# Performance work log

Hardware: AMD Instinct MI355X
Metric: run time of the kernel (lower is better)

The kernel has to match this reference:

```python
import jax, jax.numpy as jnp
import numpy as np

N = 100000   # nodes
E = 1600000  # edges (avg degree 16)
Q = 64       # mesoscale velocity bins
H = 64       # collision MLP hidden dim
DT = 0.1
REG = 1e-6


def setup_inputs() -> dict:
    key = jax.random.key(0)
    ks = jax.random.split(key, 10)
    return {
        "f": jax.random.uniform(ks[0], (N, Q), jnp.float32),
        "macro_u": jax.random.normal(ks[1], (N, 1), jnp.float32),
        "source": 0.01 * jax.random.normal(ks[2], (N, Q), jnp.float32),
        "edge_src": jax.random.randint(ks[3], (E,), 0, N, jnp.int32),
        "edge_dst": jax.random.randint(ks[4], (E,), 0, N, jnp.int32),
        "edge_w": jax.random.uniform(ks[5], (E,), jnp.float32),
        "xi": jnp.linspace(-1.0, 1.0, Q).astype(jnp.float32),
        "w_in": jax.random.normal(ks[6], (Q, H), jnp.float32) / np.float32(np.sqrt(Q)),
        "b_in": jnp.zeros((H,), jnp.float32),
        "w_hid": jax.random.normal(ks[7], (3, H, H), jnp.float32) / np.float32(np.sqrt(H)),
        "b_hid": jnp.zeros((3, H), jnp.float32),
        "w_out": jax.random.normal(ks[8], (H, Q), jnp.float32) / np.float32(np.sqrt(H)),
        "b_out": jnp.zeros((Q,), jnp.float32),
    }


def _collision(f, macro_u, xi, w_in, b_in, w_hid, b_hid, w_out, b_out):
    # 5-layer MLP: relu hidden, tanh output (CollisionOperator.forward)
    x = jax.nn.relu(f @ w_in + b_in)
    for i in range(3):  # fixed small layer count, not a data-dim loop
        x = jax.nn.relu(x @ w_hid[i] + b_hid[i])
    omega = jnp.tanh(x @ w_out + b_out)                     # [N, Q]
    # Hard collision-invariance constraint: Omega* = (I - C^T (C C^T)^-1 C) Omega
    q = f.shape[1]
    w = jnp.full((q,), 1.0 / q, f.dtype)                    # quadrature weights
    xi_shifted = xi[None, :] + macro_u                      # [N, Q]
    C = jnp.stack([jnp.broadcast_to(w, xi_shifted.shape), w * xi_shifted], axis=1)  # [N,2,Q]
    CCT = jnp.einsum('naq,nbq->nab', C, C) + REG * jnp.eye(2, dtype=f.dtype)        # [N,2,2]
    v = jnp.einsum('naq,nq->na', C, omega)                  # [N,2]
    s = jnp.linalg.solve(CCT, v[..., None])[..., 0]         # [N,2]  (== CCT^-1 v)
    return omega - jnp.einsum('naq,na->nq', C, s)           # avoid dense [N,Q,Q] projection


def _transport(f, xi, edge_src, edge_dst, edge_w, n):
    # BoltzmannUpdater.compute_transport_term: both inflow (on graph) and
    # outflow (on reverse graph) reduce to the same per-edge message
    #   m_e = (w_e / out_deg[src_e]) * xi * (f[dst_e] - f[src_e])
    # aggregated at dst (inflow) and at src (outflow); transport = outflow - inflow.
    out_deg = jax.ops.segment_sum(jnp.ones_like(edge_w), edge_src, num_segments=n)
    q_e = edge_w / out_deg[edge_src]                         # [E]
    msg = q_e[:, None] * xi[None, :] * (f[edge_dst] - f[edge_src])  # [E, Q]
    inflow = jax.ops.segment_sum(msg, edge_dst, num_segments=n)
    outflow = jax.ops.segment_sum(msg, edge_src, num_segments=n)
    return outflow - inflow


def reference(f, macro_u, source, edge_src, edge_dst, edge_w, xi,
              w_in, b_in, w_hid, b_hid, w_out, b_out):
    f = jnp.maximum(f, 0.0)  # clamp(min=0)
    omega = _collision(f, macro_u, xi, w_in, b_in, w_hid, b_hid, w_out, b_out)
    trans = _transport(f, xi, edge_src, edge_dst, edge_w, f.shape[0])
    f_new = f - DT * (trans - omega - source)
    return jnp.maximum(f_new, 0.0)
```

## Files before the change

kernel.cpp:

```cpp
#include <hip/hip_runtime.h>

#define NN 100000
#define EE 1600000
#define DTc 0.1f
#define REGc 1e-6f
#define WQc (1.0f / 64.0f)

#define NB 782
#define CHUNK 2048
#define NCH 782
#define SC_NB 598
#define MPAD (SC_NB * 1024)
#define TENT (2 * EE)
#define ACT_S 72
#define PRE_NB 6250
#define WP_NB 80
#define SIDE_BIT (1u << 24)

typedef unsigned long long u64;
typedef __attribute__((ext_vector_type(8))) short short8;
typedef __attribute__((ext_vector_type(4))) float f32x4;

__device__ __forceinline__ unsigned short f2bf(float x) {
    unsigned u = __float_as_uint(x);
    unsigned r = (u + 0x7fffu + ((u >> 16) & 1u)) >> 16;
    return (unsigned short)r;
}
__device__ __forceinline__ float bf2f(unsigned short s) {
    return __uint_as_float(((unsigned)s) << 16);
}

__global__ __launch_bounds__(256) void prep_kernel(
    const float* __restrict__ f, unsigned int* __restrict__ fb16u,
    const float* __restrict__ w_in, const float* __restrict__ w_hid,
    const float* __restrict__ w_out, unsigned short* __restrict__ wp,
    const int* __restrict__ esrc, const int* __restrict__ edst,
    int* __restrict__ bc) {
    int b = blockIdx.x;
    if (b < NCH) {
        __shared__ int cnt[NB];
        int t = threadIdx.x;
        for (int j = t; j < NB; j += 256) cnt[j] = 0;
        __syncthreads();
        int base = b * CHUNK;
        int nE = min(CHUNK, EE - base);
        int i = t * 8;
        if (i < nE) {
            int4 sa = *(const int4*)&esrc[base + i];
            int4 sb = *(const int4*)&esrc[base + i + 4];
            int4 da = *(const int4*)&edst[base + i];
            int4 db = *(const int4*)&edst[base + i + 4];
            atomicAdd(&cnt[sa.x >> 7], 1); atomicAdd(&cnt[da.x >> 7], 1);
            atomicAdd(&cnt[sa.y >> 7], 1); atomicAdd(&cnt[da.y >> 7], 1);
            atomicAdd(&cnt[sa.z >> 7], 1); atomicAdd(&cnt[da.z >> 7], 1);
            atomicAdd(&cnt[sa.w >> 7], 1); atomicAdd(&cnt[da.w >> 7], 1);
            atomicAdd(&cnt[sb.x >> 7], 1); atomicAdd(&cnt[db.x >> 7], 1);
            atomicAdd(&cnt[sb.y >> 7], 1); atomicAdd(&cnt[db.y >> 7], 1);
            atomicAdd(&cnt[sb.z >> 7], 1); atomicAdd(&cnt[db.z >> 7], 1);
            atomicAdd(&cnt[sb.w >> 7], 1); atomicAdd(&cnt[db.w >> 7], 1);
        }
        __syncthreads();
        for (int j = t; j < NB; j += 256) bc[j * NCH + b] = cnt[j];
    } else if (b < NCH + PRE_NB) {
        int i = (b - NCH) * 256 + threadIdx.x;
        float4 v = *(const float4*)&f[i * 4];
        unsigned lo = (unsigned)f2bf(fmaxf(v.x, 0.f)) | ((unsigned)f2bf(fmaxf(v.y, 0.f)) << 16);
        unsigned hi = (unsigned)f2bf(fmaxf(v.z, 0.f)) | ((unsigned)f2bf(fmaxf(v.w, 0.f)) << 16);
        fb16u[i * 2] = lo;
        fb16u[i * 2 + 1] = hi;
    } else {
        int i = (b - NCH - PRE_NB) * 256 + threadIdx.x;
        int l = i >> 12, idx = i & 4095;
        int n = idx >> 6, k = idx & 63;
        const float* W = (l == 0) ? w_in : (l < 4 ? w_hid + (l - 1) * 4096 : w_out);
        wp[i] = f2bf(W[k * 64 + n]);
    }
}

__global__ __launch_bounds__(1024) void scan_blocks(int* __restrict__ data,
                                                    int* __restrict__ bsums) {
    __shared__ int s[1024];
    int t = threadIdx.x;
    int i = blockIdx.x * 1024 + t;
    int v = data[i];
    s[t] = v;
    __syncthreads();
    for (int o = 1; o < 1024; o <<= 1) {
        int x = (t >= o) ? s[t - o] : 0;
        __syncthreads();
        s[t] += x;
        __syncthreads();
    }
    data[i] = s[t] - v;
    if (t == 0) bsums[blockIdx.x] = s[1023];
}

__global__ __launch_bounds__(1024) void scan_sums(int* __restrict__ bsums) {
    __shared__ int s[1024];
    int t = threadIdx.x;
    int v = (t < SC_NB) ? bsums[t] : 0;
    s[t] = v;
    __syncthreads();
    for (int o = 1; o < 1024; o <<= 1) {
        int x = (t >= o) ? s[t - o] : 0;
        __syncthreads();
        s[t] += x;
        __syncthreads();
    }
    if (t < SC_NB) bsums[t] = s[t] - v;
}

__global__ __launch_bounds__(256) void bin_scatter(
    const int* __restrict__ esrc, const int* __restrict__ edst,
    const float* __restrict__ ew,
    const int* __restrict__ offs, const int* __restrict__ bsums,
    u64* __restrict__ adj64) {
    __shared__ int cur[NB];
    int t = threadIdx.x, blk = blockIdx.x;
    for (int j = t; j < NB; j += 256) {
        int idx = j * NCH + blk;
        cur[j] = offs[idx] + bsums[idx >> 10];
    }
    __syncthreads();
    int base = blk * CHUNK;
    int nE = min(CHUNK, EE - base);
    int i = t * 8;
    if (i < nE) {
        int4 sa = *(const int4*)&esrc[base + i];
        int4 sb = *(const int4*)&esrc[base + i + 4];
        int4 da = *(const int4*)&edst[base + i];
        int4 db = *(const int4*)&edst[base + i + 4];
        float4 wa = *(const float4*)&ew[base + i];
        float4 wb = *(const float4*)&ew[base + i + 4];
#define EMIT(s, d, w)                                                         \
        {                                                                     \
            u64 wb64 = ((u64)__float_as_uint(w)) << 32;                       \
            int p1 = atomicAdd(&cur[(s) >> 7], 1);                            \
            adj64[p1] = wb64 | SIDE_BIT | (unsigned)((d) | (((s) & 127) << 17)); \
            int p2 = atomicAdd(&cur[(d) >> 7], 1);                            \
            adj64[p2] = wb64 | (unsigned)((s) | (((d) & 127) << 17));         \
        }
        EMIT(sa.x, da.x, wa.x) EMIT(sa.y, da.y, wa.y)
        EMIT(sa.z, da.z, wa.z) EMIT(sa.w, da.w, wa.w)
        EMIT(sb.x, db.x, wb.x) EMIT(sb.y, db.y, wb.y)
        EMIT(sb.z, db.z, wb.z) EMIT(sb.w, db.w, wb.w)
#undef EMIT
    }
}

__global__ __launch_bounds__(256) void bucket_histo(
    const int* __restrict__ offs, const int* __restrict__ bsums,
    const u64* __restrict__ adj64,
    int* __restrict__ node_offs, int* __restrict__ deg) {
    __shared__ int cnt_tot[128], cnt_src[128], sc[128];
    int t = threadIdx.x, b = blockIdx.x;
    if (t < 128) { cnt_tot[t] = 0; cnt_src[t] = 0; }
    __syncthreads();
    int i0 = b * NCH;
    int i1 = (b + 1) * NCH;
    int start = offs[i0] + bsums[i0 >> 10];
    int end = offs[i1] + bsums[i1 >> 10];
    for (int i = start + t; i < end; i += 256) {
        unsigned lo = (unsigned)adj64[i];
        int local = (lo >> 17) & 127;
        atomicAdd(&cnt_tot[local], 1);
        if (lo & SIDE_BIT) atomicAdd(&cnt_src[local], 1);
    }
    __syncthreads();
    if (t < 128) sc[t] = cnt_tot[t];
    __syncthreads();
    for (int o = 1; o < 128; o <<= 1) {
        int x = 0;
        if (t < 128 && t >= o) x = sc[t - o];
        __syncthreads();
        if (t < 128) sc[t] += x;
        __syncthreads();
    }
    if (t < 128) {
        int n = b * 128 + t;
        if (n < NN) {
            node_offs[n] = start + sc[t] - cnt_tot[t];
            deg[n] = cnt_src[t];
        }
    }
    if (b == 0 && t == 0) node_offs[NN] = TENT;
}

__global__ __launch_bounds__(256) void bucket_scatter(
    const int* __restrict__ offs, const int* __restrict__ bsums,
    const u64* __restrict__ adj64, const int* __restrict__ node_offs,
    const int* __restrict__ deg, unsigned int* __restrict__ adj4) {
    __shared__ int cur[128];
    __shared__ float ldeg[128];
    int t = threadIdx.x, b = blockIdx.x;
    if (t < 128) {
        int n = b * 128 + t;
        cur[t] = (n < NN) ? node_offs[n] : 0;
        ldeg[t] = (n < NN) ? (float)deg[n] : 1.f;
    }
    __syncthreads();
    int i0 = b * NCH;
    int i1 = (b + 1) * NCH;
    int start = offs[i0] + bsums[i0 >> 10];
    int end = offs[i1] + bsums[i1 >> 10];
    for (int i = start + t; i < end; i += 256) {
        u64 e = adj64[i];
        unsigned lo = (unsigned)e;
        int local = (lo >> 17) & 127;
        unsigned other = lo & 0x1FFFFu;
        float w = __uint_as_float((unsigned)(e >> 32));
        float dv = (lo & SIDE_BIT) ? ldeg[local] : (float)deg[other];
        float q = w / dv;
        unsigned q15 = (unsigned)(q * 32768.f + 0.5f);
        if (q15 > 32767u) q15 = 32767u;
        int p = atomicAdd(&cur[local], 1);
        adj4[p] = (q15 << 17) | other;
    }
}

#define ACC8(q, r)                                          \
    a0 = fmaf(q, __uint_as_float(r.x << 16), a0);           \
    a1 = fmaf(q, __uint_as_float(r.x & 0xFFFF0000u), a1);   \
    a2 = fmaf(q, __uint_as_float(r.y << 16), a2);           \
    a3 = fmaf(q, __uint_as_float(r.y & 0xFFFF0000u), a3);   \
    a4 = fmaf(q, __uint_as_float(r.z << 16), a4);           \
    a5 = fmaf(q, __uint_as_float(r.z & 0xFFFF0000u), a5);   \
    a6 = fmaf(q, __uint_as_float(r.w << 16), a6);           \
    a7 = fmaf(q, __uint_as_float(r.w & 0xFFFF0000u), a7);   \
    qs += q;

__global__ __launch_bounds__(256) void gather_kernel(
    const unsigned int* __restrict__ fb16u, const int* __restrict__ node_offs,
    const unsigned int* __restrict__ adj, const float* __restrict__ xi,
    float* __restrict__ trans) {
    const float QS = 1.f / 32768.f;
    int lane = threadIdx.x & 63;
    int n = blockIdx.x * 4 + (threadIdx.x >> 6);
    if (n >= NN) return;
    int c = lane & 7;
    int qt = lane >> 3;
    int j = node_offs[n];
    int end = node_offs[n + 1];
    float a0 = 0.f, a1 = 0.f, a2 = 0.f, a3 = 0.f;
    float a4 = 0.f, a5 = 0.f, a6 = 0.f, a7 = 0.f, qs = 0.f;
    for (; j + 32 <= end; j += 32) {
        unsigned e0 = __builtin_nontemporal_load(&adj[j + qt]);
        unsigned e1 = __builtin_nontemporal_load(&adj[j + 8 + qt]);
        unsigned e2 = __builtin_nontemporal_load(&adj[j + 16 + qt]);
        unsigned e3 = __builtin_nontemporal_load(&adj[j + 24 + qt]);
        uint4 r0 = *(const uint4*)&fb16u[(e0 & 0x1FFFFu) * 32 + c * 4];
        uint4 r1 = *(const uint4*)&fb16u[(e1 & 0x1FFFFu) * 32 + c * 4];
        uint4 r2 = *(const uint4*)&fb16u[(e2 & 0x1FFFFu) * 32 + c * 4];
        uint4 r3 = *(const uint4*)&fb16u[(e3 & 0x1FFFFu) * 32 + c * 4];
        float q0 = (float)(e0 >> 17) * QS;
        float q1 = (float)(e1 >> 17) * QS;
        float q2 = (float)(e2 >> 17) * QS;
        float q3 = (float)(e3 >> 17) * QS;
        ACC8(q0, r0)
        ACC8(q1, r1)
        ACC8(q2, r2)
        ACC8(q3, r3)
    }
    for (; j + 8 <= end; j += 8) {
        unsigned e = __builtin_nontemporal_load(&adj[j + qt]);
        uint4 r = *(const uint4*)&fb16u[(e & 0x1FFFFu) * 32 + c * 4];
        float q = (float)(e >> 17) * QS;
        ACC8(q, r)
    }
    if (j < end) {
        int idx = j + qt;
        bool ok = idx < end;
        unsigned e = ok ? adj[idx] : 0u;
        uint4 r = *(const uint4*)&fb16u[(e & 0x1FFFFu) * 32 + c * 4];
        float q = ok ? (float)(e >> 17) * QS : 0.f;
        ACC8(q, r)
    }
#define RED3(x) x += __shfl_xor(x, 8); x += __shfl_xor(x, 16); x += __shfl_xor(x, 32)
    RED3(a0); RED3(a1); RED3(a2); RED3(a3);
    RED3(a4); RED3(a5); RED3(a6); RED3(a7); RED3(qs);
    if (qt == 0) {
        uint4 rn = *(const uint4*)&fb16u[n * 32 + c * 4];
        float4 x0 = *(const float4*)&xi[c * 8];
        float4 x1 = *(const float4*)&xi[c * 8 + 4];
        f32x4 o0, o1;
        o0.x = x0.x * (a0 - qs * __uint_as_float(rn.x << 16));
        o0.y = x0.y * (a1 - qs * __uint_as_float(rn.x & 0xFFFF0000u));
        o0.z = x0.z * (a2 - qs * __uint_as_float(rn.y << 16));
        o0.w = x0.w * (a3 - qs * __uint_as_float(rn.y & 0xFFFF0000u));
        o1.x = x1.x * (a4 - qs * __uint_as_float(rn.z << 16));
        o1.y = x1.y * (a5 - qs * __uint_as_float(rn.z & 0xFFFF0000u));
        o1.z = x1.z * (a6 - qs * __uint_as_float(rn.w << 16));
        o1.w = x1.w * (a7 - qs * __uint_as_float(rn.w & 0xFFFF0000u));
        __builtin_nontemporal_store(o0, (f32x4*)&trans[n * 64 + c * 8]);
        __builtin_nontemporal_store(o1, (f32x4*)&trans[n * 64 + c * 8 + 4]);
    }
}

__global__ __launch_bounds__(256) void node_kernel(
    const unsigned short* __restrict__ fb16, const float* __restrict__ f,
    const float* __restrict__ macro_u, const float* __restrict__ source,
    const float* __restrict__ xi, const unsigned short* __restrict__ wp,
    const float* __restrict__ b_in, const float* __restrict__ b_hid,
    const float* __restrict__ b_out,
    const float* __restrict__ trans, float* __restrict__ out) {
    __shared__ __attribute__((aligned(16))) unsigned short act[128 * ACT_S];
    __shared__ float s0s[128], s1s[128], us[128], xif[64];

    const int t = threadIdx.x;
    const int wid = t >> 6;
    const int lane = t & 63;
    const int m = lane & 15;
    const int quad = lane >> 4;
    const int nodeBase = blockIdx.x * 128;
    const int gbase = nodeBase * 64;

    if (t < 128) {
        int n = nodeBase + t;
        us[t] = (n < NN) ? macro_u[n] : 0.f;
    }
    if (t < 64) xif[t] = xi[t];

#pragma unroll
    for (int i = 0; i < 8; i++) {
        int r = wid * 32 + i * 4 + (lane >> 4);
        int c = (lane & 15) * 4;
        uint2 v = {0u, 0u};
        if (nodeBase + r < NN) v = *(const uint2*)&fb16[gbase + r * 64 + c];
        *(uint2*)&act[r * ACT_S + c] = v;
    }

    const int rowbase = wid * 32;

    for (int l = 0; l < 5; l++) {
        const unsigned short* W = wp + l * 4096;
        const float* B = (l == 0) ? b_in : (l < 4 ? b_hid + (l - 1) * 64 : b_out);

        short8 Af[2][2], Bf[4][2];
#pragma unroll
        for (int rt = 0; rt < 2; rt++)
#pragma unroll
            for (int kk = 0; kk < 2; kk++)
                Af[rt][kk] = *(const short8*)&act[(rowbase + rt * 16 + m) * ACT_S + kk * 32 + quad * 8];
#pragma unroll
        for (int ct = 0; ct < 4; ct++)
#pragma unroll
            for (int kk = 0; kk < 2; kk++)
                Bf[ct][kk] = *(const short8*)&W[(ct * 16 + m) * 64 + kk * 32 + quad * 8];

        f32x4 acc[2][4];
#pragma unroll
        for (int rt = 0; rt < 2; rt++)
#pragma unroll
            for (int ct = 0; ct < 4; ct++) {
                acc[rt][ct] = (f32x4){0.f, 0.f, 0.f, 0.f};
                acc[rt][ct] = __builtin_amdgcn_mfma_f32_16x16x32_bf16(Af[rt][0], Bf[ct][0], acc[rt][ct], 0, 0, 0);
                acc[rt][ct] = __builtin_amdgcn_mfma_f32_16x16x32_bf16(Af[rt][1], Bf[ct][1], acc[rt][ct], 0, 0, 0);
            }

#pragma unroll
        for (int rt = 0; rt < 2; rt++)
#pragma unroll
            for (int ct = 0; ct < 4; ct++) {
                float bv = B[ct * 16 + m];
#pragma unroll
                for (int r = 0; r < 4; r++) {
                    int row = rowbase + rt * 16 + quad * 4 + r;
                    float val = acc[rt][ct][r] + bv;
                    val = (l < 4) ? fmaxf(val, 0.f) : tanhf(val);
                    act[row * ACT_S + ct * 16 + m] = f2bf(val);
                }
            }
    }
    __syncthreads();

    if (t < 128) {
        float u = us[t];
        float v0 = 0.f, v1 = 0.f, sxs2 = 0.f, sxi = 0.f;
        const short8* rp = (const short8*)&act[t * ACT_S];
#pragma unroll
        for (int c = 0; c < 8; c++) {
            short8 v = rp[c];
#pragma unroll
            for (int jj = 0; jj < 8; jj++) {
                float om = bf2f((unsigned short)v[jj]);
                float xv = xif[c * 8 + jj];
                float xs = xv + u;
                v0 += om;
                v1 += xs * om;
                sxs2 += xs * xs;
                sxi += xv;
            }
        }
        v0 *= WQc;
        v1 *= WQc;
        float c00 = WQc + REGc;
        float c01 = WQc * WQc * (sxi + 64.f * u);
        float c11 = WQc * WQc * sxs2 + REGc;
        float det = c00 * c11 - c01 * c01;
        float inv = 1.0f / det;
        s0s[t] = (c11 * v0 - c01 * v1) * inv;
        s1s[t] = (c00 * v1 - c01 * v0) * inv;
    }
    __syncthreads();

#pragma unroll
    for (int i = 0; i < 8; i++) {
        int e = (i * 256 + t) * 4;
        int nl = e >> 6;
        if (nodeBase + nl < NN) {
            int g = gbase + e;
            int c0 = e & 63;
            float4 fv = *(const float4*)&f[g];
            float4 sv = *(const float4*)&source[g];
            float4 tv = *(const float4*)&trans[g];
            float uu = us[nl];
            float sv0 = s0s[nl], sv1 = s1s[nl];
            float4 ov;
            float* ovp = (float*)&ov;
            const float* fp = (const float*)&fv;
            const float* sp = (const float*)&sv;
            const float* tp = (const float*)&tv;
#pragma unroll
            for (int jj = 0; jj < 4; jj++) {
                float om = bf2f(act[nl * ACT_S + c0 + jj]);
                float xs = xif[c0 + jj] + uu;
                float omst = om - WQc * (sv0 + xs * sv1);
                float val = fmaxf(fp[jj], 0.f) + DTc * (sp[jj] + omst - tp[jj]);
                ovp[jj] = fmaxf(val, 0.f);
            }
            *(float4*)&out[g] = ov;
        }
    }
}

extern "C" void kernel_launch(void* const* d_in, const int* in_sizes, int n_in,
                              void* d_out, int out_size, void* d_ws, size_t ws_size,
                              hipStream_t stream) {
    const float* f       = (const float*)d_in[0];
    const float* macro_u = (const float*)d_in[1];
    const float* source  = (const float*)d_in[2];
    const int*   esrc    = (const int*)d_in[3];
    const int*   edst    = (const int*)d_in[4];
    const float* ew      = (const float*)d_in[5];
    const float* xi      = (const float*)d_in[6];
    const float* w_in    = (const float*)d_in[7];
    const float* b_in    = (const float*)d_in[8];
    const float* w_hid   = (const float*)d_in[9];
    const float* b_hid   = (const float*)d_in[10];
    const float* w_out   = (const float*)d_in[11];
    const float* b_out   = (const float*)d_in[12];
    float* out = (float*)d_out;

    u64* adj64 = (u64*)d_ws;
    unsigned int* adj4 = (unsigned int*)(adj64 + TENT);
    int* deg   = (int*)(adj4 + TENT);
    int* bc    = deg + NN;
    int* bsums = bc + MPAD;
    int* node_offs = bsums + 1024;
    float* trans = (float*)(node_offs + NN + 8);
    unsigned short* fb16 = (unsigned short*)(trans + (size_t)NN * 64);
    unsigned short* wp = fb16 + (size_t)NN * 64;

    hipMemsetAsync(bc, 0, (size_t)MPAD * sizeof(int), stream);

    prep_kernel<<<NCH + PRE_NB + WP_NB, 256, 0, stream>>>(
        f, (unsigned int*)fb16, w_in, w_hid, w_out, wp, esrc, edst, bc);
    scan_blocks<<<SC_NB, 1024, 0, stream>>>(bc, bsums);
    scan_sums<<<1, 1024, 0, stream>>>(bsums);
    bin_scatter<<<NCH, 256, 0, stream>>>(esrc, edst, ew, bc, bsums, adj64);
    bucket_histo<<<NB, 256, 0, stream>>>(bc, bsums, adj64, node_offs, deg);
    bucket_scatter<<<NB, 256, 0, stream>>>(bc, bsums, adj64, node_offs, deg, adj4);
    gather_kernel<<<(NN + 3) / 4, 256, 0, stream>>>((const unsigned int*)fb16,
                                                    node_offs, adj4, xi, trans);
    node_kernel<<<(NN + 127) / 128, 256, 0, stream>>>(
        fb16, f, macro_u, source, xi, wp, b_in, b_hid, b_out, trans, out);
}
```

Before: 336.4 us.

## Replace global bin-count scan with fixed-capacity buckets and atomic bucket cursors

Removes the separate per-chunk histogram pass, the 600K-entry memset and the two-level scan. bin_scatter now counts locally, reserves space in each 128-node bucket via one global atomic per bucket, and writes into fixed-capacity (CAP) slots; a single small scan over 782 bucket totals yields compact offsets for node_offs. The bf16 prep also writes 16-byte vectors. Risk: a bucket exceeding CAP entries would overflow, and edge order within buckets becomes nondeterministic.

New measurement: 336.8 us. No clear change (+0.1%).

```diff
diff --git a/kernel.cpp b/kernel.cpp
--- a/kernel.cpp
+++ b/kernel.cpp
@@ -7,13 +7,11 @@
 #define WQc (1.0f / 64.0f)
 
 #define NB 782
-#define CHUNK 2048
-#define NCH 782
-#define SC_NB 598
-#define MPAD (SC_NB * 1024)
+#define CAP 4736
+#define BS_NB 782
 #define TENT (2 * EE)
 #define ACT_S 72
-#define PRE_NB 6250
+#define PRE_NB 3125
 #define WP_NB 80
 #define SIDE_BIT (1u << 24)
 
@@ -29,47 +27,27 @@
 __device__ __forceinline__ float bf2f(unsigned short s) {
     return __uint_as_float(((unsigned)s) << 16);
 }
+__device__ __forceinline__ unsigned pack2(float a, float b) {
+    return (unsigned)f2bf(fmaxf(a, 0.f)) | ((unsigned)f2bf(fmaxf(b, 0.f)) << 16);
+}
 
 __global__ __launch_bounds__(256) void prep_kernel(
     const float* __restrict__ f, unsigned int* __restrict__ fb16u,
     const float* __restrict__ w_in, const float* __restrict__ w_hid,
-    const float* __restrict__ w_out, unsigned short* __restrict__ wp,
-    const int* __restrict__ esrc, const int* __restrict__ edst,
-    int* __restrict__ bc) {
+    const float* __restrict__ w_out, unsigned short* __restrict__ wp) {
     int b = blockIdx.x;
-    if (b < NCH) {
-        __shared__ int cnt[NB];
-        int t = threadIdx.x;
-        for (int j = t; j < NB; j += 256) cnt[j] = 0;
-        __syncthreads();
-        int base = b * CHUNK;
-        int nE = min(CHUNK, EE - base);
-        int i = t * 8;
-        if (i < nE) {
-            int4 sa = *(const int4*)&esrc[base + i];
-            int4 sb = *(const int4*)&esrc[base + i + 4];
-            int4 da = *(const int4*)&edst[base + i];
-            int4 db = *(const int4*)&edst[base + i + 4];
-            atomicAdd(&cnt[sa.x >> 7], 1); atomicAdd(&cnt[da.x >> 7], 1);
-            atomicAdd(&cnt[sa.y >> 7], 1); atomicAdd(&cnt[da.y >> 7], 1);
-            atomicAdd(&cnt[sa.z >> 7], 1); atomicAdd(&cnt[da.z >> 7], 1);
-            atomicAdd(&cnt[sa.w >> 7], 1); atomicAdd(&cnt[da.w >> 7], 1);
-            atomicAdd(&cnt[sb.x >> 7], 1); atomicAdd(&cnt[db.x >> 7], 1);
-            atomicAdd(&cnt[sb.y >> 7], 1); atomicAdd(&cnt[db.y >> 7], 1);
-            atomicAdd(&cnt[sb.z >> 7], 1); atomicAdd(&cnt[db.z >> 7], 1);
-            atomicAdd(&cnt[sb.w >> 7], 1); atomicAdd(&cnt[db.w >> 7], 1);
-        }
-        __syncthreads();
-        for (int j = t; j < NB; j += 256) bc[j * NCH + b] = cnt[j];
-    } else if (b < NCH + PRE_NB) {
-        int i = (b - NCH) * 256 + threadIdx.x;
-        float4 v = *(const float4*)&f[i * 4];
-        unsigned lo = (unsigned)f2bf(fmaxf(v.x, 0.f)) | ((unsigned)f2bf(fmaxf(v.y, 0.f)) << 16);
-        unsigned hi = (unsigned)f2bf(fmaxf(v.z, 0.f)) | ((unsigned)f2bf(fmaxf(v.w, 0.f)) << 16);
-        fb16u[i * 2] = lo;
-        fb16u[i * 2 + 1] = hi;
+    if (b < PRE_NB) {
+        int i = b * 256 + threadIdx.x;
+        float4 v0 = *(const float4*)&f[i * 8];
+        float4 v1 = *(const float4*)&f[i * 8 + 4];
+        uint4 w;
+        w.x = pack2(v0.x, v0.y);
+        w.y = pack2(v0.z, v0.w);
+        w.z = pack2(v1.x, v1.y);
+        w.w = pack2(v1.z, v1.w);
+        *(uint4*)&fb16u[i * 4] = w;
     } else {
-        int i = (b - NCH - PRE_NB) * 256 + threadIdx.x;
+        int i = (b - PRE_NB) * 256 + threadIdx.x;
         int l = i >> 12, idx = i & 4095;
         int n = idx >> 6, k = idx & 63;
         const float* W = (l == 0) ? w_in : (l < 4 ? w_hid + (l - 1) * 4096 : w_out);
@@ -77,67 +55,51 @@
     }
 }
 
-__global__ __launch_bounds__(1024) void scan_blocks(int* __restrict__ data,
-                                                    int* __restrict__ bsums) {
-    __shared__ int s[1024];
-    int t = threadIdx.x;
-    int i = blockIdx.x * 1024 + t;
-    int v = data[i];
-    s[t] = v;
-    __syncthreads();
-    for (int o = 1; o < 1024; o <<= 1) {
-        int x = (t >= o) ? s[t - o] : 0;
-        __syncthreads();
-        s[t] += x;
-        __syncthreads();
-    }
-    data[i] = s[t] - v;
-    if (t == 0) bsums[blockIdx.x] = s[1023];
-}
-
-__global__ __launch_bounds__(1024) void scan_sums(int* __restrict__ bsums) {
-    __shared__ int s[1024];
-    int t = threadIdx.x;
-    int v = (t < SC_NB) ? bsums[t] : 0;
-    s[t] = v;
-    __syncthreads();
-    for (int o = 1; o < 1024; o <<= 1) {
-        int x = (t >= o) ? s[t - o] : 0;
-        __syncthreads();
-        s[t] += x;
-        __syncthreads();
-    }
-    if (t < SC_NB) bsums[t] = s[t] - v;
-}
-
 __global__ __launch_bounds__(256) void bin_scatter(
     const int* __restrict__ esrc, const int* __restrict__ edst,
-    const float* __restrict__ ew,
-    const int* __restrict__ offs, const int* __restrict__ bsums,
+    const float* __restrict__ ew, int* __restrict__ bcur,
     u64* __restrict__ adj64) {
-    __shared__ int cur[NB];
+    __shared__ int cnt[NB];
+    __shared__ int bas[NB];
     int t = threadIdx.x, blk = blockIdx.x;
+    for (int j = t; j < NB; j += 256) cnt[j] = 0;
+    __syncthreads();
+    int base = blk * 2048;
+    int nE = min(2048, EE - base);
+    int i = t * 8;
+    bool act = (i < nE);
+    int4 sa, sb, da, db;
+    float4 wa, wb;
+    if (act) {
+        sa = *(const int4*)&esrc[base + i];
+        sb = *(const int4*)&esrc[base + i + 4];
+        da = *(const int4*)&edst[base + i];
+        db = *(const int4*)&edst[base + i + 4];
+        wa = *(const float4*)&ew[base + i];
+        wb = *(const float4*)&ew[base + i + 4];
+        atomicAdd(&cnt[sa.x >> 7], 1); atomicAdd(&cnt[da.x >> 7], 1);
+        atomicAdd(&cnt[sa.y >> 7], 1); atomicAdd(&cnt[da.y >> 7], 1);
+        atomicAdd(&cnt[sa.z >> 7], 1); atomicAdd(&cnt[da.z >> 7], 1);
+        atomicAdd(&cnt[sa.w >> 7], 1); atomicAdd(&cnt[da.w >> 7], 1);
+        atomicAdd(&cnt[sb.x >> 7], 1); atomicAdd(&cnt[db.x >> 7], 1);
+        atomicAdd(&cnt[sb.y >> 7], 1); atomicAdd(&cnt[db.y >> 7], 1);
+        atomicAdd(&cnt[sb.z >> 7], 1); atomicAdd(&cnt[db.z >> 7], 1);
+        atomicAdd(&cnt[sb.w >> 7], 1); atomicAdd(&cnt[db.w >> 7], 1);
+    }
+    __syncthreads();
     for (int j = t; j < NB; j += 256) {
-        int idx = j * NCH + blk;
-        cur[j] = offs[idx] + bsums[idx >> 10];
-    }
-    __syncthreads();
-    int base = blk * CHUNK;
-    int nE = min(CHUNK, EE - base);
-    int i = t * 8;
-    if (i < nE) {
-        int4 sa = *(const int4*)&esrc[base + i];
-        int4 sb = *(const int4*)&esrc[base + i + 4];
-        int4 da = *(const int4*)&edst[base + i];
-        int4 db = *(const int4*)&edst[base + i + 4];
-        float4 wa = *(const float4*)&ew[base + i];
-        float4 wb = *(const float4*)&ew[base + i + 4];
+        int c = cnt[j];
+        bas[j] = (c ? atomicAdd(&bcur[j], c) : 0) + j * CAP;
+        cnt[j] = 0;
+    }
+    __syncthreads();
+    if (act) {
 #define EMIT(s, d, w)                                                         \
         {                                                                     \
             u64 wb64 = ((u64)__float_as_uint(w)) << 32;                       \
-            int p1 = atomicAdd(&cur[(s) >> 7], 1);                            \
+            int p1 = bas[(s) >> 7] + atomicAdd(&cnt[(s) >> 7], 1);            \
             adj64[p1] = wb64 | SIDE_BIT | (unsigned)((d) | (((s) & 127) << 17)); \
-            int p2 = atomicAdd(&cur[(d) >> 7], 1);                            \
+            int p2 = bas[(d) >> 7] + atomicAdd(&cnt[(d) >> 7], 1);            \
             adj64[p2] = wb64 | (unsigned)((s) | (((d) & 127) << 17));         \
         }
         EMIT(sa.x, da.x, wa.x) EMIT(sa.y, da.y, wa.y)
@@ -148,20 +110,34 @@
     }
 }
 
+__global__ __launch_bounds__(1024) void scan_nb(const int* __restrict__ bcur,
+                                                int* __restrict__ cbase) {
+    __shared__ int s[1024];
+    int t = threadIdx.x;
+    int v = (t < NB) ? bcur[t] : 0;
+    s[t] = v;
+    __syncthreads();
+    for (int o = 1; o < 1024; o <<= 1) {
+        int x = (t >= o) ? s[t - o] : 0;
+        __syncthreads();
+        s[t] += x;
+        __syncthreads();
+    }
+    if (t < NB) cbase[t] = s[t] - v;
+}
+
 __global__ __launch_bounds__(256) void bucket_histo(
-    const int* __restrict__ offs, const int* __restrict__ bsums,
+    const int* __restrict__ bcur, const int* __restrict__ cbase,
     const u64* __restrict__ adj64,
     int* __restrict__ node_offs, int* __restrict__ deg) {
     __shared__ int cnt_tot[128], cnt_src[128], sc[128];
     int t = threadIdx.x, b = blockIdx.x;
     if (t < 128) { cnt_tot[t] = 0; cnt_src[t] = 0; }
     __syncthreads();
-    int i0 = b * NCH;
-    int i1 = (b + 1) * NCH;
-    int start = offs[i0] + bsums[i0 >> 10];
-    int end = offs[i1] + bsums[i1 >> 10];
-    for (int i = start + t; i < end; i += 256) {
-        unsigned lo = (unsigned)adj64[i];
+    int used = bcur[b];
+    int gstart = b * CAP;
+    for (int i = t; i < used; i += 256) {
+        unsigned lo = (unsigned)adj64[gstart + i];
         int local = (lo >> 17) & 127;
         atomicAdd(&cnt_tot[local], 1);
         if (lo & SIDE_BIT) atomicAdd(&cnt_src[local], 1);
@@ -179,7 +155,7 @@
     if (t < 128) {
         int n = b * 128 + t;
         if (n < NN) {
-            node_offs[n] = start + sc[t] - cnt_tot[t];
+            node_offs[n] = cbase[b] + sc[t] - cnt_tot[t];
             deg[n] = cnt_src[t];
         }
     }
@@ -187,9 +163,9 @@
 }
 
 __global__ __launch_bounds__(256) void bucket_scatter(
-    const int* __restrict__ offs, const int* __restrict__ bsums,
-    const u64* __restrict__ adj64, const int* __restrict__ node_offs,
-    const int* __restrict__ deg, unsigned int* __restrict__ adj4) {
+    const int* __restrict__ bcur, const u64* __restrict__ adj64,
+    const int* __restrict__ node_offs, const int* __restrict__ deg,
+    unsigned int* __restrict__ adj4) {
     __shared__ int cur[128];
     __shared__ float ldeg[128];
     int t = threadIdx.x, b = blockIdx.x;
@@ -199,12 +175,10 @@
         ldeg[t] = (n < NN) ? (float)deg[n] : 1.f;
     }
     __syncthreads();
-    int i0 = b * NCH;
-    int i1 = (b + 1) * NCH;
-    int start = offs[i0] + bsums[i0 >> 10];
-    int end = offs[i1] + bsums[i1 >> 10];
-    for (int i = start + t; i < end; i += 256) {
-        u64 e = adj64[i];
+    int used = bcur[b];
+    int gstart = b * CAP;
+    for (int i = t; i < used; i += 256) {
+        u64 e = adj64[gstart + i];
         unsigned lo = (unsigned)e;
         int local = (lo >> 17) & 127;
         unsigned other = lo & 0x1FFFFu;
@@ -452,24 +426,23 @@
     float* out = (float*)d_out;
 
     u64* adj64 = (u64*)d_ws;
-    unsigned int* adj4 = (unsigned int*)(adj64 + TENT);
+    unsigned int* adj4 = (unsigned int*)(adj64 + (size_t)NB * CAP);
     int* deg   = (int*)(adj4 + TENT);
-    int* bc    = deg + NN;
-    int* bsums = bc + MPAD;
-    int* node_offs = bsums + 1024;
+    int* bcur  = deg + NN;
+    int* cbase = bcur + 784;
+    int* node_offs = cbase + 784;
     float* trans = (float*)(node_offs + NN + 8);
     unsigned short* fb16 = (unsigned short*)(trans + (size_t)NN * 64);
     unsigned short* wp = fb16 + (size_t)NN * 64;
 
-    hipMemsetAsync(bc, 0, (size_t)MPAD * sizeof(int), stream);
-
-    prep_kernel<<<NCH + PRE_NB + WP_NB, 256, 0, stream>>>(
-        f, (unsigned int*)fb16, w_in, w_hid, w_out, wp, esrc, edst, bc);
-    scan_blocks<<<SC_NB, 1024, 0, stream>>>(bc, bsums);
-    scan_sums<<<1, 1024, 0, stream>>>(bsums);
-    bin_scatter<<<NCH, 256, 0, stream>>>(esrc, edst, ew, bc, bsums, adj64);
-    bucket_histo<<<NB, 256, 0, stream>>>(bc, bsums, adj64, node_offs, deg);
-    bucket_scatter<<<NB, 256, 0, stream>>>(bc, bsums, adj64, node_offs, deg, adj4);
+    hipMemsetAsync(bcur, 0, 784 * sizeof(int), stream);
+
+    prep_kernel<<<PRE_NB + WP_NB, 256, 0, stream>>>(
+        f, (unsigned int*)fb16, w_in, w_hid, w_out, wp);
+    bin_scatter<<<BS_NB, 256, 0, stream>>>(esrc, edst, ew, bcur, adj64);
+    scan_nb<<<1, 1024, 0, stream>>>(bcur, cbase);
+    bucket_histo<<<NB, 256, 0, stream>>>(bcur, cbase, adj64, node_offs, deg);
+    bucket_scatter<<<NB, 256, 0, stream>>>(bcur, adj64, node_offs, deg, adj4);
     gather_kernel<<<(NN + 3) / 4, 256, 0, stream>>>((const unsigned int*)fb16,
                                                     node_offs, adj4, xi, trans);
     node_kernel<<<(NN + 127) / 128, 256, 0, stream>>>(
```
